# Optimization experiments

Measured on AMD Instinct MI355X. Metric: run time of the kernel, lower is better.

## Reference

```python
import jax, jax.numpy as jnp
import numpy as np

NUM_HEADS = 4
KERNEL = 4
EPS = 1e-6


def _causal_conv1d(x, w, b):
    # x: (B,S,D), w: (D,1,K) depthwise, b: (D,)
    xc = x.transpose(0, 2, 1)  # (B,D,S)
    y = jax.lax.conv_general_dilated(
        xc, w, window_strides=(1,), padding=[(w.shape[-1] - 1, 0)],
        feature_group_count=xc.shape[1])
    return (y + b[None, :, None]).transpose(0, 2, 1)  # (B,S,D)


def _headwise(x, w):
    # x: (B,S,D), w: (NH, DH_out, DH_in) block-diagonal linear, no bias
    B, S, D = x.shape
    nh, dout, din = w.shape
    xh = x.reshape(B, S, nh, din)
    return jnp.einsum('bshd,hod->bsho', xh, w).reshape(B, S, nh * dout)


def _slstm_scan(gates, R, b):
    # gates: (B,S,4,NH,DH) ordered [i,f,z,o]; R: (NH,DH,4*DH); b: (4,NH,DH)
    B, S, _, nh, dh = gates.shape
    gseq = gates.transpose(1, 0, 2, 3, 4)  # (S,B,4,NH,DH)
    zero = jnp.zeros((B, nh, dh), gates.dtype)
    init = (zero, zero, zero, zero)  # h, c, n, m

    def step(carry, g):
        h, c, n, m = carry
        rec = jnp.einsum('bhd,hdk->bhk', h, R)
        rec = rec.reshape(B, nh, 4, dh).transpose(0, 2, 1, 3)  # (B,4,NH,DH)
        raw = g + rec + b[None]
        iraw, fraw, zraw, oraw = raw[:, 0], raw[:, 1], raw[:, 2], raw[:, 3]
        logfplusm = m + jax.nn.log_sigmoid(fraw)
        m_new = jnp.maximum(iraw, logfplusm)  # stabilizer
        ig = jnp.exp(iraw - m_new)
        fg = jnp.exp(logfplusm - m_new)
        c_new = fg * c + ig * jnp.tanh(zraw)
        n_new = fg * n + ig
        h_new = jax.nn.sigmoid(oraw) * c_new / n_new
        return (h_new, c_new, n_new, m_new), h_new

    _, ys = jax.lax.scan(step, init, gseq)  # ys: (S,B,NH,DH)
    return ys.transpose(1, 2, 0, 3)  # (B,NH,S,DH)


def _multihead_layernorm(y, scale, bias):
    # y: (B,NH,S,DH); normalize over DH per head
    mu = y.mean(-1, keepdims=True)
    var = y.var(-1, keepdims=True)
    yn = (y - mu) * jax.lax.rsqrt(var + EPS)
    nh, dh = y.shape[1], y.shape[3]
    return yn * scale.reshape(1, nh, 1, dh) + bias.reshape(1, nh, 1, dh)


def setup_inputs() -> dict:
    key = jax.random.key(0)
    ks = jax.random.split(key, 12)
    B, S, D = 4, 2048, 1024
    nh, dh = NUM_HEADS, D // NUM_HEADS
    sd_conv = 1.0 / np.sqrt(KERNEL)
    sd_head = 1.0 / np.sqrt(dh)
    return {
        'x': jax.random.normal(ks[0], (B, S, D), jnp.float32),
        'conv_w': jax.random.normal(ks[1], (D, 1, KERNEL), jnp.float32) * sd_conv,
        'conv_b': jnp.zeros((D,), jnp.float32),
        'w_i': jax.random.normal(ks[2], (nh, dh, dh), jnp.float32) * sd_head,
        'w_f': jax.random.normal(ks[3], (nh, dh, dh), jnp.float32) * sd_head,
        'w_z': jax.random.normal(ks[4], (nh, dh, dh), jnp.float32) * sd_head,
        'w_o': jax.random.normal(ks[5], (nh, dh, dh), jnp.float32) * sd_head,
        'rec_kernel': jax.random.normal(ks[6], (nh, dh, 4 * dh), jnp.float32) * sd_head,
        'cell_bias': jnp.zeros((4, nh, dh), jnp.float32),
        'gn_scale': jnp.ones((D,), jnp.float32),
        'gn_bias': jnp.zeros((D,), jnp.float32),
    }


def reference(x, conv_w, conv_b, w_i, w_f, w_z, w_o, rec_kernel, cell_bias, gn_scale, gn_bias):
    B, S, D = x.shape
    dh = D // NUM_HEADS
    x_conv = jax.nn.swish(_causal_conv1d(x, conv_w, conv_b))
    i = _headwise(x_conv, w_i)
    f = _headwise(x_conv, w_f)
    z = _headwise(x, w_z)
    o = _headwise(x, w_o)
    # concat order [i,f,z,o]; reshape to (B,S,4,NH,DH)
    gates = jnp.stack([i, f, z, o], axis=2).reshape(B, S, 4, NUM_HEADS, dh)
    y = _slstm_scan(gates, rec_kernel, cell_bias)  # (B,NH,S,DH)
    out = _multihead_layernorm(y, gn_scale, gn_bias)
    return out.transpose(0, 2, 1, 3).reshape(B, S, D)
```

## Files before the change

kernel.cpp:

```cpp
#include <hip/hip_runtime.h>
#include <hip/hip_bf16.h>

#define NH 4
#define DH 256
#define DMODEL 1024
#define BB 4
#define SS 2048

typedef __attribute__((ext_vector_type(4))) float f32x4;
typedef __attribute__((ext_vector_type(8))) short bf16x8;
typedef __attribute__((ext_vector_type(4))) int i32x4;

__device__ __forceinline__ int dot4i8(int acc, int a, int b) {
#if __has_builtin(__builtin_amdgcn_sdot4)
    return __builtin_amdgcn_sdot4(a, b, acc, false);
#else
#pragma unroll
    for (int i = 0; i < 4; ++i) {
        int av = (a << (24 - 8 * i)) >> 24;
        int bv = (b << (24 - 8 * i)) >> 24;
        acc += av * bv;
    }
    return acc;
#endif
}

__global__ void k_conv(const float* __restrict__ x, const float* __restrict__ cw,
                       const float* __restrict__ cb, float* __restrict__ xc) {
    int bs = blockIdx.x;
    int s = bs & (SS - 1);
    const float* xrow = x + (size_t)bs * DMODEL;
#pragma unroll
    for (int dd = 0; dd < 4; ++dd) {
        int d = threadIdx.x + dd * 256;
        float w0 = cw[d * 4 + 0], w1 = cw[d * 4 + 1], w2 = cw[d * 4 + 2], w3 = cw[d * 4 + 3];
        float acc = cb[d] + w3 * xrow[d];
        if (s >= 1) acc += w2 * xrow[d - DMODEL];
        if (s >= 2) acc += w1 * xrow[d - 2 * DMODEL];
        if (s >= 3) acc += w0 * xrow[d - 3 * DMODEL];
        float sig = 1.f / (1.f + __expf(-acc));
        xc[(size_t)bs * DMODEL + d] = acc * sig;
    }
}

__global__ void k_gemm(const float* __restrict__ x, const float* __restrict__ xc,
                       const float* __restrict__ wi, const float* __restrict__ wf,
                       const float* __restrict__ wz, const float* __restrict__ wo,
                       float* __restrict__ gates) {
    int h = blockIdx.z >> 1, pair = blockIdx.z & 1;
    const float* A = pair ? x : xc;
    int n0 = blockIdx.y * 64;
    const float* W = (n0 < 256) ? (pair ? wz : wi) : (pair ? wo : wf);
    int nl = n0 & 255;
    int m0 = blockIdx.x * 64;

    __shared__ __align__(16) __hip_bfloat16 Al[64][72];
    __shared__ __align__(16) __hip_bfloat16 Bl[64][72];

    int tid = threadIdx.x;
    int lane = tid & 63, wv = tid >> 6;
    f32x4 acc[4] = {};

    for (int k0 = 0; k0 < 256; k0 += 64) {
        __syncthreads();
#pragma unroll
        for (int i = 0; i < 4; ++i) {
            int f4 = tid + i * 256;
            int r = f4 >> 4, c4 = (f4 & 15) * 4;
            const float* srcA = A + (size_t)(m0 + r) * DMODEL + h * DH + k0 + c4;
            float4 v = *(const float4*)srcA;
            Al[r][c4 + 0] = __float2bfloat16(v.x);
            Al[r][c4 + 1] = __float2bfloat16(v.y);
            Al[r][c4 + 2] = __float2bfloat16(v.z);
            Al[r][c4 + 3] = __float2bfloat16(v.w);
            const float* srcB = W + (size_t)(h * DH + nl + r) * DH + k0 + c4;
            float4 u = *(const float4*)srcB;
            Bl[r][c4 + 0] = __float2bfloat16(u.x);
            Bl[r][c4 + 1] = __float2bfloat16(u.y);
            Bl[r][c4 + 2] = __float2bfloat16(u.z);
            Bl[r][c4 + 3] = __float2bfloat16(u.w);
        }
        __syncthreads();
#pragma unroll
        for (int kk = 0; kk < 64; kk += 32) {
            bf16x8 a = *(const bf16x8*)&Al[wv * 16 + (lane & 15)][kk + (lane >> 4) * 8];
#pragma unroll
            for (int nt = 0; nt < 4; ++nt) {
                bf16x8 bfr = *(const bf16x8*)&Bl[nt * 16 + (lane & 15)][kk + (lane >> 4) * 8];
                acc[nt] = __builtin_amdgcn_mfma_f32_16x16x32_bf16(a, bfr, acc[nt], 0, 0, 0);
            }
        }
    }
#pragma unroll
    for (int nt = 0; nt < 4; ++nt)
#pragma unroll
        for (int r = 0; r < 4; ++r) {
            int m = m0 + wv * 16 + (lane >> 4) * 4 + r;
            int n = n0 + nt * 16 + (lane & 15);
            int b = m >> 11, s = m & (SS - 1);
            int g = pair * 2 + (n >> 8), d = n & 255;
            gates[((((size_t)(b * NH + h)) * SS + s) * 4 + g) * DH + d] = acc[nt][r];
        }
}

__global__ void k_prep(const float* __restrict__ R, int* __restrict__ Wq,
                       float* __restrict__ scales) {
    int colid = blockIdx.x * 4 + (threadIdx.x >> 6);
    int lane = threadIdx.x & 63;
    int h = colid >> 10, k = colid & 1023;
    const float* base = R + (size_t)h * 256 * 1024 + k;
    float v[4];
    float mx = 0.f;
#pragma unroll
    for (int i = 0; i < 4; ++i) {
        v[i] = base[(size_t)(lane * 4 + i) * 1024];
        mx = fmaxf(mx, fabsf(v[i]));
    }
    for (int off = 32; off; off >>= 1) mx = fmaxf(mx, __shfl_xor(mx, off));
    mx = fmaxf(mx, 1e-30f);
    float scale = mx * (1.f / 127.f);
    float inv = 127.f / mx;
    int pk = 0;
#pragma unroll
    for (int i = 0; i < 4; ++i) {
        int q = (int)rintf(v[i] * inv);
        q = max(-127, min(127, q));
        pk |= (q & 255) << (8 * i);
    }
    Wq[(h * 64 + lane) * 1024 + k] = pk;
    if (lane == 0) scales[h * 1024 + k] = scale;
}

__launch_bounds__(1024, 4)
__global__ void k_scan(const float* __restrict__ gates, const int* __restrict__ Wq,
                       const float* __restrict__ scales, const float* __restrict__ bias,
                       float* __restrict__ y) {
    int bh = blockIdx.x;
    int h = bh & 3;
    int t = threadIdx.x;

    __shared__ __align__(16) signed char hq[256];
    __shared__ float rec[1024];

    int w[64];
#pragma unroll
    for (int j = 0; j < 64; ++j) w[j] = Wq[(h * 64 + j) * 1024 + t];
    float colmul = scales[h * 1024 + t] * (1.f / 127.f);

    float c = 0.f, n = 0.f, mstate = 0.f;
    float bi = 0.f, bf_ = 0.f, bz = 0.f, bo = 0.f;
    int d = t;
    if (t < 256) {
        bi = bias[(0 * NH + h) * DH + d];
        bf_ = bias[(1 * NH + h) * DH + d];
        bz = bias[(2 * NH + h) * DH + d];
        bo = bias[(3 * NH + h) * DH + d];
    }
    if (t < 16) ((i32x4*)hq)[t] = (i32x4){0, 0, 0, 0};
    const float* gbase = gates + (size_t)bh * SS * 1024;
    float* ybase = y + (size_t)bh * SS * DH;
    __syncthreads();

    for (int s = 0; s < SS; ++s) {
        float gi = 0.f, gf = 0.f, gz = 0.f, go = 0.f;
        if (t < 256) {
            const float* gp = gbase + (size_t)s * 1024 + d;
            gi = gp[0]; gf = gp[256]; gz = gp[512]; go = gp[768];
        }
        int acc = 0;
#pragma unroll
        for (int g4 = 0; g4 < 4; ++g4) {
            i32x4 h0 = ((const i32x4*)hq)[g4 * 4 + 0];
            i32x4 h1 = ((const i32x4*)hq)[g4 * 4 + 1];
            i32x4 h2 = ((const i32x4*)hq)[g4 * 4 + 2];
            i32x4 h3 = ((const i32x4*)hq)[g4 * 4 + 3];
            acc = dot4i8(acc, w[g4 * 16 + 0], h0.x);
            acc = dot4i8(acc, w[g4 * 16 + 1], h0.y);
            acc = dot4i8(acc, w[g4 * 16 + 2], h0.z);
            acc = dot4i8(acc, w[g4 * 16 + 3], h0.w);
            acc = dot4i8(acc, w[g4 * 16 + 4], h1.x);
            acc = dot4i8(acc, w[g4 * 16 + 5], h1.y);
            acc = dot4i8(acc, w[g4 * 16 + 6], h1.z);
            acc = dot4i8(acc, w[g4 * 16 + 7], h1.w);
            acc = dot4i8(acc, w[g4 * 16 + 8], h2.x);
            acc = dot4i8(acc, w[g4 * 16 + 9], h2.y);
            acc = dot4i8(acc, w[g4 * 16 + 10], h2.z);
            acc = dot4i8(acc, w[g4 * 16 + 11], h2.w);
            acc = dot4i8(acc, w[g4 * 16 + 12], h3.x);
            acc = dot4i8(acc, w[g4 * 16 + 13], h3.y);
            acc = dot4i8(acc, w[g4 * 16 + 14], h3.z);
            acc = dot4i8(acc, w[g4 * 16 + 15], h3.w);
        }
        rec[t] = (float)acc * colmul;
        __syncthreads();
        if (t < 256) {
            float ri = rec[d], rf = rec[256 + d], rz = rec[512 + d], ro = rec[768 + d];
            float rawi = gi + ri + bi;
            float rawf = gf + rf + bf_;
            float rawz = gz + rz + bz;
            float rawo = go + ro + bo;
            float lsf = fminf(rawf, 0.f) - __logf(1.f + __expf(-fabsf(rawf)));
            float lfm = mstate + lsf;
            float mn = fmaxf(rawi, lfm);
            float ig = __expf(rawi - mn);
            float fg = __expf(lfm - mn);
            float az = fabsf(rawz);
            float e2 = __expf(-2.f * az);
            float th = (1.f - e2) / (1.f + e2);
            th = rawz < 0.f ? -th : th;
            c = fg * c + ig * th;
            n = fg * n + ig;
            mstate = mn;
            float so = 1.f / (1.f + __expf(-rawo));
            float hv = so * c / n;
            ybase[(size_t)s * DH + d] = hv;
            int q = (int)rintf(hv * 127.f);
            hq[d] = (signed char)q;
        }
        __syncthreads();
    }
}

__global__ void k_ln(const float* __restrict__ y, const float* __restrict__ gsc,
                     const float* __restrict__ gbi, float* __restrict__ out) {
    int bid = blockIdx.x;
    int s = bid & (SS - 1);
    int bh = bid >> 11;
    int b = bh >> 2, h = bh & 3;
    int d = threadIdx.x;
    float v = y[(size_t)bid * DH + d];
    float s1 = v, s2 = v * v;
    for (int off = 32; off; off >>= 1) {
        s1 += __shfl_xor(s1, off);
        s2 += __shfl_xor(s2, off);
    }
    __shared__ float a1[4], a2[4];
    int wv = threadIdx.x >> 6, ln = threadIdx.x & 63;
    if (ln == 0) { a1[wv] = s1; a2[wv] = s2; }
    __syncthreads();
    s1 = a1[0] + a1[1] + a1[2] + a1[3];
    s2 = a2[0] + a2[1] + a2[2] + a2[3];
    float mu = s1 * (1.f / 256.f);
    float var = s2 * (1.f / 256.f) - mu * mu;
    float rs = rsqrtf(var + 1e-6f);
    float o = (v - mu) * rs * gsc[h * DH + d] + gbi[h * DH + d];
    out[((size_t)(b * SS + s)) * DMODEL + h * DH + d] = o;
}

extern "C" void kernel_launch(void* const* d_in, const int* in_sizes, int n_in,
                              void* d_out, int out_size, void* d_ws, size_t ws_size,
                              hipStream_t stream) {
    (void)in_sizes; (void)n_in; (void)out_size; (void)ws_size;
    const float* x = (const float*)d_in[0];
    const float* cw = (const float*)d_in[1];
    const float* cb = (const float*)d_in[2];
    const float* wi = (const float*)d_in[3];
    const float* wf = (const float*)d_in[4];
    const float* wz = (const float*)d_in[5];
    const float* wo = (const float*)d_in[6];
    const float* R = (const float*)d_in[7];
    const float* cbias = (const float*)d_in[8];
    const float* gsc = (const float*)d_in[9];
    const float* gbi = (const float*)d_in[10];
    float* out = (float*)d_out;

    char* ws = (char*)d_ws;
    float* xc = (float*)ws;
    float* gates = (float*)(ws + 33554432ull);
    float* yb = (float*)(ws + 167772160ull);
    int* Wq = (int*)(ws + 201326592ull);
    float* scales = (float*)(ws + 202375168ull);

    k_prep<<<1024, 256, 0, stream>>>(R, Wq, scales);
    k_conv<<<BB * SS, 256, 0, stream>>>(x, cw, cb, xc);
    k_gemm<<<dim3(128, 8, 8), 256, 0, stream>>>(x, xc, wi, wf, wz, wo, gates);
    k_scan<<<16, 1024, 0, stream>>>(gates, Wq, scales, cbias, yb);
    k_ln<<<BB * SS * NH, 256, 0, stream>>>(yb, gsc, gbi, out);
}
```

Baseline: 2.107 ms.

## Interleave gate layout, prefetch next-step gates, split dot chains, lighten scan barriers

The GEMM epilogue now writes gates interleaved per channel as [d][4 gates], so the scan can load all four gates with one float4 per step. The scan loop also prefetches the next timestep's gates into registers a step ahead, to hide global load latency behind the recurrent dot products. The 64-long serial sdot4 chain is split into four independent accumulators to shorten the dependency chain. __syncthreads is replaced with a custom barrier that waits only on LDS counters (lgkmcnt), so the prefetched global load does not stall at the barrier. This relies on the barrier not needing vmcnt for correctness and changes the gate memory layout in two kernels together.

```diff
diff --git a/kernel.cpp b/kernel.cpp
--- a/kernel.cpp
+++ b/kernel.cpp
@@ -23,6 +23,13 @@
     }
     return acc;
 #endif
+}
+
+__device__ __forceinline__ void wg_barrier() {
+    __builtin_amdgcn_sched_barrier(0);
+    asm volatile("s_waitcnt lgkmcnt(0)" ::: "memory");
+    __builtin_amdgcn_s_barrier();
+    __builtin_amdgcn_sched_barrier(0);
 }
 
 __global__ void k_conv(const float* __restrict__ x, const float* __restrict__ cw,
@@ -99,7 +106,7 @@
             int n = n0 + nt * 16 + (lane & 15);
             int b = m >> 11, s = m & (SS - 1);
             int g = pair * 2 + (n >> 8), d = n & 255;
-            gates[((((size_t)(b * NH + h)) * SS + s) * 4 + g) * DH + d] = acc[nt][r];
+            gates[((((size_t)(b * NH + h)) * SS + s) * DH + d) * 4 + g] = acc[nt][r];
         }
 }
 
@@ -149,7 +156,7 @@
 
     float c = 0.f, n = 0.f, mstate = 0.f;
     float bi = 0.f, bf_ = 0.f, bz = 0.f, bo = 0.f;
-    int d = t;
+    int d = t & 255;
     if (t < 256) {
         bi = bias[(0 * NH + h) * DH + d];
         bf_ = bias[(1 * NH + h) * DH + d];
@@ -157,48 +164,51 @@
         bo = bias[(3 * NH + h) * DH + d];
     }
     if (t < 16) ((i32x4*)hq)[t] = (i32x4){0, 0, 0, 0};
-    const float* gbase = gates + (size_t)bh * SS * 1024;
+    const float4* gp = (const float4*)(gates + (size_t)bh * SS * 1024) + d;
     float* ybase = y + (size_t)bh * SS * DH;
     __syncthreads();
 
+    float4 gc = {0.f, 0.f, 0.f, 0.f};
+    if (t < 256) gc = gp[0];
+
     for (int s = 0; s < SS; ++s) {
-        float gi = 0.f, gf = 0.f, gz = 0.f, go = 0.f;
-        if (t < 256) {
-            const float* gp = gbase + (size_t)s * 1024 + d;
-            gi = gp[0]; gf = gp[256]; gz = gp[512]; go = gp[768];
-        }
-        int acc = 0;
+        float4 gn = gc;
+        if (t < 256 && s + 1 < SS) gn = gp[(size_t)(s + 1) * 256];
+
+        int accs[4];
 #pragma unroll
         for (int g4 = 0; g4 < 4; ++g4) {
             i32x4 h0 = ((const i32x4*)hq)[g4 * 4 + 0];
             i32x4 h1 = ((const i32x4*)hq)[g4 * 4 + 1];
             i32x4 h2 = ((const i32x4*)hq)[g4 * 4 + 2];
             i32x4 h3 = ((const i32x4*)hq)[g4 * 4 + 3];
-            acc = dot4i8(acc, w[g4 * 16 + 0], h0.x);
-            acc = dot4i8(acc, w[g4 * 16 + 1], h0.y);
-            acc = dot4i8(acc, w[g4 * 16 + 2], h0.z);
-            acc = dot4i8(acc, w[g4 * 16 + 3], h0.w);
-            acc = dot4i8(acc, w[g4 * 16 + 4], h1.x);
-            acc = dot4i8(acc, w[g4 * 16 + 5], h1.y);
-            acc = dot4i8(acc, w[g4 * 16 + 6], h1.z);
-            acc = dot4i8(acc, w[g4 * 16 + 7], h1.w);
-            acc = dot4i8(acc, w[g4 * 16 + 8], h2.x);
-            acc = dot4i8(acc, w[g4 * 16 + 9], h2.y);
-            acc = dot4i8(acc, w[g4 * 16 + 10], h2.z);
-            acc = dot4i8(acc, w[g4 * 16 + 11], h2.w);
-            acc = dot4i8(acc, w[g4 * 16 + 12], h3.x);
-            acc = dot4i8(acc, w[g4 * 16 + 13], h3.y);
-            acc = dot4i8(acc, w[g4 * 16 + 14], h3.z);
-            acc = dot4i8(acc, w[g4 * 16 + 15], h3.w);
-        }
-        rec[t] = (float)acc * colmul;
-        __syncthreads();
+            int a = 0;
+            a = dot4i8(a, w[g4 * 16 + 0], h0.x);
+            a = dot4i8(a, w[g4 * 16 + 1], h0.y);
+            a = dot4i8(a, w[g4 * 16 + 2], h0.z);
+            a = dot4i8(a, w[g4 * 16 + 3], h0.w);
+            a = dot4i8(a, w[g4 * 16 + 4], h1.x);
+            a = dot4i8(a, w[g4 * 16 + 5], h1.y);
+            a = dot4i8(a, w[g4 * 16 + 6], h1.z);
+            a = dot4i8(a, w[g4 * 16 + 7], h1.w);
+            a = dot4i8(a, w[g4 * 16 + 8], h2.x);
+            a = dot4i8(a, w[g4 * 16 + 9], h2.y);
+            a = dot4i8(a, w[g4 * 16 + 10], h2.z);
+            a = dot4i8(a, w[g4 * 16 + 11], h2.w);
+            a = dot4i8(a, w[g4 * 16 + 12], h3.x);
+            a = dot4i8(a, w[g4 * 16 + 13], h3.y);
+            a = dot4i8(a, w[g4 * 16 + 14], h3.z);
+            a = dot4i8(a, w[g4 * 16 + 15], h3.w);
+            accs[g4] = a;
+        }
+        rec[t] = (float)(accs[0] + accs[1] + accs[2] + accs[3]) * colmul;
+        wg_barrier();
         if (t < 256) {
             float ri = rec[d], rf = rec[256 + d], rz = rec[512 + d], ro = rec[768 + d];
-            float rawi = gi + ri + bi;
-            float rawf = gf + rf + bf_;
-            float rawz = gz + rz + bz;
-            float rawo = go + ro + bo;
+            float rawi = gc.x + ri + bi;
+            float rawf = gc.y + rf + bf_;
+            float rawz = gc.z + rz + bz;
+            float rawo = gc.w + ro + bo;
             float lsf = fminf(rawf, 0.f) - __logf(1.f + __expf(-fabsf(rawf)));
             float lfm = mstate + lsf;
             float mn = fmaxf(rawi, lfm);
@@ -217,7 +227,8 @@
             int q = (int)rintf(hv * 127.f);
             hq[d] = (signed char)q;
         }
-        __syncthreads();
+        gc = gn;
+        wg_barrier();
     }
 }
 
```

Result: slower. 2.246 ms (+6.6%).

## Restructure sLSTM scan: quad-split K reduction, double-buffered h, one barrier per step

Applied to the files above, without the earlier changes.

The recurrent scan now assigns four threads per hidden unit. Each thread computes a quarter of the K-dimension dot product for all four gates, and the partial sums are combined with DPP quad reductions instead of staging them in a shared `rec` array. The hidden state is double-buffered in LDS, which cuts the per-step sync to a single lightweight barrier. The next step's gate inputs are prefetched into registers. Every thread now runs the redundant elementwise cell math, and the barrier relies on a custom lgkmcnt wait.

```diff
diff --git a/kernel.cpp b/kernel.cpp
--- a/kernel.cpp
+++ b/kernel.cpp
@@ -23,6 +23,17 @@
     }
     return acc;
 #endif
+}
+
+__device__ __forceinline__ void wg_barrier() {
+    asm volatile("s_waitcnt lgkmcnt(0)" ::: "memory");
+    __builtin_amdgcn_s_barrier();
+}
+
+__device__ __forceinline__ int quad_reduce_add(int v) {
+    v += __builtin_amdgcn_update_dpp(0, v, 0xB1, 0xF, 0xF, true);
+    v += __builtin_amdgcn_update_dpp(0, v, 0x4E, 0xF, 0xF, true);
+    return v;
 }
 
 __global__ void k_conv(const float* __restrict__ x, const float* __restrict__ cw,
@@ -131,93 +142,106 @@
     if (lane == 0) scales[h * 1024 + k] = scale;
 }
 
-__launch_bounds__(1024, 4)
+__launch_bounds__(1024, 1)
 __global__ void k_scan(const float* __restrict__ gates, const int* __restrict__ Wq,
                        const float* __restrict__ scales, const float* __restrict__ bias,
                        float* __restrict__ y) {
     int bh = blockIdx.x;
     int h = bh & 3;
     int t = threadIdx.x;
-
-    __shared__ __align__(16) signed char hq[256];
-    __shared__ float rec[1024];
-
-    int w[64];
-#pragma unroll
-    for (int j = 0; j < 64; ++j) w[j] = Wq[(h * 64 + j) * 1024 + t];
-    float colmul = scales[h * 1024 + t] * (1.f / 127.f);
+    int d = t >> 2, q = t & 3;
+
+    __shared__ __align__(16) signed char hq[2][256];
+
+    int w[4][16];
+#pragma unroll
+    for (int g = 0; g < 4; ++g)
+#pragma unroll
+        for (int j = 0; j < 16; ++j)
+            w[g][j] = Wq[(h * 64 + q * 16 + j) * 1024 + g * 256 + d];
+
+    float colmul[4];
+#pragma unroll
+    for (int g = 0; g < 4; ++g)
+        colmul[g] = scales[h * 1024 + g * 256 + d] * (1.f / 127.f);
+
+    float bi = bias[(0 * NH + h) * DH + d];
+    float bf_ = bias[(1 * NH + h) * DH + d];
+    float bz = bias[(2 * NH + h) * DH + d];
+    float bo = bias[(3 * NH + h) * DH + d];
 
     float c = 0.f, n = 0.f, mstate = 0.f;
-    float bi = 0.f, bf_ = 0.f, bz = 0.f, bo = 0.f;
-    int d = t;
-    if (t < 256) {
-        bi = bias[(0 * NH + h) * DH + d];
-        bf_ = bias[(1 * NH + h) * DH + d];
-        bz = bias[(2 * NH + h) * DH + d];
-        bo = bias[(3 * NH + h) * DH + d];
-    }
-    if (t < 16) ((i32x4*)hq)[t] = (i32x4){0, 0, 0, 0};
-    const float* gbase = gates + (size_t)bh * SS * 1024;
-    float* ybase = y + (size_t)bh * SS * DH;
+    const float* gbase = gates + (size_t)bh * SS * 1024 + d;
+    float* ybase = y + (size_t)bh * SS * DH + d;
+
+    if (t < 32) ((i32x4*)hq)[t] = (i32x4){0, 0, 0, 0};
     __syncthreads();
 
+    float gcx = gbase[0], gcy = gbase[256], gcz = gbase[512], gcw = gbase[768];
+
+    int p = 0;
     for (int s = 0; s < SS; ++s) {
-        float gi = 0.f, gf = 0.f, gz = 0.f, go = 0.f;
-        if (t < 256) {
-            const float* gp = gbase + (size_t)s * 1024 + d;
-            gi = gp[0]; gf = gp[256]; gz = gp[512]; go = gp[768];
-        }
-        int acc = 0;
-#pragma unroll
-        for (int g4 = 0; g4 < 4; ++g4) {
-            i32x4 h0 = ((const i32x4*)hq)[g4 * 4 + 0];
-            i32x4 h1 = ((const i32x4*)hq)[g4 * 4 + 1];
-            i32x4 h2 = ((const i32x4*)hq)[g4 * 4 + 2];
-            i32x4 h3 = ((const i32x4*)hq)[g4 * 4 + 3];
-            acc = dot4i8(acc, w[g4 * 16 + 0], h0.x);
-            acc = dot4i8(acc, w[g4 * 16 + 1], h0.y);
-            acc = dot4i8(acc, w[g4 * 16 + 2], h0.z);
-            acc = dot4i8(acc, w[g4 * 16 + 3], h0.w);
-            acc = dot4i8(acc, w[g4 * 16 + 4], h1.x);
-            acc = dot4i8(acc, w[g4 * 16 + 5], h1.y);
-            acc = dot4i8(acc, w[g4 * 16 + 6], h1.z);
-            acc = dot4i8(acc, w[g4 * 16 + 7], h1.w);
-            acc = dot4i8(acc, w[g4 * 16 + 8], h2.x);
-            acc = dot4i8(acc, w[g4 * 16 + 9], h2.y);
-            acc = dot4i8(acc, w[g4 * 16 + 10], h2.z);
-            acc = dot4i8(acc, w[g4 * 16 + 11], h2.w);
-            acc = dot4i8(acc, w[g4 * 16 + 12], h3.x);
-            acc = dot4i8(acc, w[g4 * 16 + 13], h3.y);
-            acc = dot4i8(acc, w[g4 * 16 + 14], h3.z);
-            acc = dot4i8(acc, w[g4 * 16 + 15], h3.w);
-        }
-        rec[t] = (float)acc * colmul;
-        __syncthreads();
-        if (t < 256) {
-            float ri = rec[d], rf = rec[256 + d], rz = rec[512 + d], ro = rec[768 + d];
-            float rawi = gi + ri + bi;
-            float rawf = gf + rf + bf_;
-            float rawz = gz + rz + bz;
-            float rawo = go + ro + bo;
-            float lsf = fminf(rawf, 0.f) - __logf(1.f + __expf(-fabsf(rawf)));
-            float lfm = mstate + lsf;
-            float mn = fmaxf(rawi, lfm);
-            float ig = __expf(rawi - mn);
-            float fg = __expf(lfm - mn);
-            float az = fabsf(rawz);
-            float e2 = __expf(-2.f * az);
-            float th = (1.f - e2) / (1.f + e2);
-            th = rawz < 0.f ? -th : th;
-            c = fg * c + ig * th;
-            n = fg * n + ig;
-            mstate = mn;
-            float so = 1.f / (1.f + __expf(-rawo));
-            float hv = so * c / n;
-            ybase[(size_t)s * DH + d] = hv;
-            int q = (int)rintf(hv * 127.f);
-            hq[d] = (signed char)q;
-        }
-        __syncthreads();
+        float gnx = gcx, gny = gcy, gnz = gcz, gnw = gcw;
+        if (s + 1 < SS) {
+            const float* gp = gbase + (size_t)(s + 1) * 1024;
+            gnx = gp[0]; gny = gp[256]; gnz = gp[512]; gnw = gp[768];
+        }
+
+        const i32x4* hv4 = (const i32x4*)hq[p];
+        i32x4 h0 = hv4[q * 4 + 0];
+        i32x4 h1 = hv4[q * 4 + 1];
+        i32x4 h2 = hv4[q * 4 + 2];
+        i32x4 h3 = hv4[q * 4 + 3];
+        int hdw[16];
+        hdw[0] = h0.x; hdw[1] = h0.y; hdw[2] = h0.z; hdw[3] = h0.w;
+        hdw[4] = h1.x; hdw[5] = h1.y; hdw[6] = h1.z; hdw[7] = h1.w;
+        hdw[8] = h2.x; hdw[9] = h2.y; hdw[10] = h2.z; hdw[11] = h2.w;
+        hdw[12] = h3.x; hdw[13] = h3.y; hdw[14] = h3.z; hdw[15] = h3.w;
+
+        int acc[4] = {0, 0, 0, 0};
+#pragma unroll
+        for (int g = 0; g < 4; ++g)
+#pragma unroll
+            for (int j = 0; j < 16; ++j)
+                acc[g] = dot4i8(acc[g], w[g][j], hdw[j]);
+
+        acc[0] = quad_reduce_add(acc[0]);
+        acc[1] = quad_reduce_add(acc[1]);
+        acc[2] = quad_reduce_add(acc[2]);
+        acc[3] = quad_reduce_add(acc[3]);
+
+        float ri = (float)acc[0] * colmul[0];
+        float rf = (float)acc[1] * colmul[1];
+        float rz = (float)acc[2] * colmul[2];
+        float ro = (float)acc[3] * colmul[3];
+
+        float rawi = gcx + ri + bi;
+        float rawf = gcy + rf + bf_;
+        float rawz = gcz + rz + bz;
+        float rawo = gcw + ro + bo;
+        float lsf = fminf(rawf, 0.f) - __logf(1.f + __expf(-fabsf(rawf)));
+        float lfm = mstate + lsf;
+        float mn = fmaxf(rawi, lfm);
+        float ig = __expf(rawi - mn);
+        float fg = __expf(lfm - mn);
+        float az = fabsf(rawz);
+        float e2 = __expf(-2.f * az);
+        float th = (1.f - e2) / (1.f + e2);
+        th = rawz < 0.f ? -th : th;
+        c = fg * c + ig * th;
+        n = fg * n + ig;
+        mstate = mn;
+        float so = 1.f / (1.f + __expf(-rawo));
+        float hv = so * c / n;
+
+        if (q == 0) {
+            ybase[(size_t)s * DH] = hv;
+            hq[p ^ 1][d] = (signed char)(int)rintf(hv * 127.f);
+        }
+
+        gcx = gnx; gcy = gny; gcz = gnz; gcw = gnw;
+        p ^= 1;
+        wg_barrier();
     }
 }
 
```

Result: slower. 2.967 ms (+40.8%).

## Restructure sLSTM scan to 512 threads with lane-pair DPP exchange and one barrier

Applied to the files above, without the earlier changes.

The recurrent scan kernel now runs 512 threads per block, each computing two gate columns, so lane pairs hold all four gates for one hidden unit. The gates are exchanged with a DPP xor-1 swizzle instead of going through shared memory. A double-buffered quantized h vector removes one of the two workgroup barriers per step, and gate inputs are prefetched two steps ahead. The aim is to shorten the serial per-step critical path. The cost is twice the register-resident weights per thread and redundant activation math on both lanes of each pair.

```diff
diff --git a/kernel.cpp b/kernel.cpp
--- a/kernel.cpp
+++ b/kernel.cpp
@@ -23,6 +23,16 @@
     }
     return acc;
 #endif
+}
+
+__device__ __forceinline__ void wg_barrier() {
+    asm volatile("s_waitcnt lgkmcnt(0)" ::: "memory");
+    __builtin_amdgcn_s_barrier();
+}
+
+__device__ __forceinline__ float xor1_f32(float v) {
+    int r = __builtin_amdgcn_update_dpp(0, __float_as_int(v), 0xB1, 0xF, 0xF, true);
+    return __int_as_float(r);
 }
 
 __global__ void k_conv(const float* __restrict__ x, const float* __restrict__ cw,
@@ -131,94 +141,94 @@
     if (lane == 0) scales[h * 1024 + k] = scale;
 }
 
-__launch_bounds__(1024, 4)
+__launch_bounds__(512, 2)
 __global__ void k_scan(const float* __restrict__ gates, const int* __restrict__ Wq,
                        const float* __restrict__ scales, const float* __restrict__ bias,
                        float* __restrict__ y) {
     int bh = blockIdx.x;
     int h = bh & 3;
     int t = threadIdx.x;
-
-    __shared__ __align__(16) signed char hq[256];
-    __shared__ float rec[1024];
-
-    int w[64];
-#pragma unroll
-    for (int j = 0; j < 64; ++j) w[j] = Wq[(h * 64 + j) * 1024 + t];
-    float colmul = scales[h * 1024 + t] * (1.f / 127.f);
+    int d = t >> 1, pair = t & 1;
+
+    __shared__ __align__(16) signed char hq[2][256];
+
+    int col0 = pair * 256 + d;
+    int col1 = col0 + 512;
+
+    int w0[64], w1[64];
+#pragma unroll
+    for (int j = 0; j < 64; ++j) {
+        w0[j] = Wq[(h * 64 + j) * 1024 + col0];
+        w1[j] = Wq[(h * 64 + j) * 1024 + col1];
+    }
+    float cm0 = scales[h * 1024 + col0] * (1.f / 127.f);
+    float cm1 = scales[h * 1024 + col1] * (1.f / 127.f);
+    float b0 = bias[(pair * NH + h) * DH + d];
+    float b1 = bias[((2 + pair) * NH + h) * DH + d];
 
     float c = 0.f, n = 0.f, mstate = 0.f;
-    float bi = 0.f, bf_ = 0.f, bz = 0.f, bo = 0.f;
-    int d = t;
-    if (t < 256) {
-        bi = bias[(0 * NH + h) * DH + d];
-        bf_ = bias[(1 * NH + h) * DH + d];
-        bz = bias[(2 * NH + h) * DH + d];
-        bo = bias[(3 * NH + h) * DH + d];
-    }
-    if (t < 16) ((i32x4*)hq)[t] = (i32x4){0, 0, 0, 0};
     const float* gbase = gates + (size_t)bh * SS * 1024;
-    float* ybase = y + (size_t)bh * SS * DH;
+    float* ybase = y + (size_t)bh * SS * DH + d;
+
+    if (t < 32) ((i32x4*)hq)[t] = (i32x4){0, 0, 0, 0};
     __syncthreads();
 
-    for (int s = 0; s < SS; ++s) {
-        float gi = 0.f, gf = 0.f, gz = 0.f, go = 0.f;
-        if (t < 256) {
-            const float* gp = gbase + (size_t)s * 1024 + d;
-            gi = gp[0]; gf = gp[256]; gz = gp[512]; go = gp[768];
-        }
-        int acc = 0;
-#pragma unroll
-        for (int g4 = 0; g4 < 4; ++g4) {
-            i32x4 h0 = ((const i32x4*)hq)[g4 * 4 + 0];
-            i32x4 h1 = ((const i32x4*)hq)[g4 * 4 + 1];
-            i32x4 h2 = ((const i32x4*)hq)[g4 * 4 + 2];
-            i32x4 h3 = ((const i32x4*)hq)[g4 * 4 + 3];
-            acc = dot4i8(acc, w[g4 * 16 + 0], h0.x);
-            acc = dot4i8(acc, w[g4 * 16 + 1], h0.y);
-            acc = dot4i8(acc, w[g4 * 16 + 2], h0.z);
-            acc = dot4i8(acc, w[g4 * 16 + 3], h0.w);
-            acc = dot4i8(acc, w[g4 * 16 + 4], h1.x);
-            acc = dot4i8(acc, w[g4 * 16 + 5], h1.y);
-            acc = dot4i8(acc, w[g4 * 16 + 6], h1.z);
-            acc = dot4i8(acc, w[g4 * 16 + 7], h1.w);
-            acc = dot4i8(acc, w[g4 * 16 + 8], h2.x);
-            acc = dot4i8(acc, w[g4 * 16 + 9], h2.y);
-            acc = dot4i8(acc, w[g4 * 16 + 10], h2.z);
-            acc = dot4i8(acc, w[g4 * 16 + 11], h2.w);
-            acc = dot4i8(acc, w[g4 * 16 + 12], h3.x);
-            acc = dot4i8(acc, w[g4 * 16 + 13], h3.y);
-            acc = dot4i8(acc, w[g4 * 16 + 14], h3.z);
-            acc = dot4i8(acc, w[g4 * 16 + 15], h3.w);
-        }
-        rec[t] = (float)acc * colmul;
-        __syncthreads();
-        if (t < 256) {
-            float ri = rec[d], rf = rec[256 + d], rz = rec[512 + d], ro = rec[768 + d];
-            float rawi = gi + ri + bi;
-            float rawf = gf + rf + bf_;
-            float rawz = gz + rz + bz;
-            float rawo = go + ro + bo;
-            float lsf = fminf(rawf, 0.f) - __logf(1.f + __expf(-fabsf(rawf)));
-            float lfm = mstate + lsf;
-            float mn = fmaxf(rawi, lfm);
-            float ig = __expf(rawi - mn);
-            float fg = __expf(lfm - mn);
-            float az = fabsf(rawz);
-            float e2 = __expf(-2.f * az);
-            float th = (1.f - e2) / (1.f + e2);
-            th = rawz < 0.f ? -th : th;
-            c = fg * c + ig * th;
-            n = fg * n + ig;
-            mstate = mn;
-            float so = 1.f / (1.f + __expf(-rawo));
-            float hv = so * c / n;
-            ybase[(size_t)s * DH + d] = hv;
-            int q = (int)rintf(hv * 127.f);
-            hq[d] = (signed char)q;
-        }
-        __syncthreads();
-    }
+    float gA0 = gbase[col0], gA1 = gbase[col1];
+    float gB0 = gbase[1024 + col0], gB1 = gbase[1024 + col1];
+
+#define SCAN_STEP(P, G0, G1, SCUR)                                            \
+    {                                                                          \
+        int acc0 = 0, acc1 = 0;                                                \
+        const i32x4* hv4 = (const i32x4*)hq[P];                                \
+        _Pragma("unroll") for (int kb = 0; kb < 4; ++kb) {                     \
+            i32x4 ha = hv4[kb * 4 + 0];                                        \
+            i32x4 hb = hv4[kb * 4 + 1];                                        \
+            i32x4 hc = hv4[kb * 4 + 2];                                        \
+            i32x4 hd_ = hv4[kb * 4 + 3];                                       \
+            int hd[16] = {ha.x, ha.y, ha.z, ha.w, hb.x, hb.y, hb.z, hb.w,      \
+                          hc.x, hc.y, hc.z, hc.w, hd_.x, hd_.y, hd_.z, hd_.w}; \
+            _Pragma("unroll") for (int j = 0; j < 16; ++j) {                   \
+                acc0 = dot4i8(acc0, w0[kb * 16 + j], hd[j]);                   \
+                acc1 = dot4i8(acc1, w1[kb * 16 + j], hd[j]);                   \
+            }                                                                  \
+        }                                                                      \
+        float rawA = G0 + (float)acc0 * cm0 + b0;                              \
+        float rawB = G1 + (float)acc1 * cm1 + b1;                              \
+        int sp = (SCUR) + 2 < SS ? (SCUR) + 2 : SS - 1;                        \
+        G0 = gbase[(size_t)sp * 1024 + col0];                                  \
+        G1 = gbase[(size_t)sp * 1024 + col1];                                  \
+        float recvA = xor1_f32(rawA);                                          \
+        float recvB = xor1_f32(rawB);                                          \
+        float rawi = pair ? recvA : rawA;                                      \
+        float rawf = pair ? rawA : recvA;                                      \
+        float rawz = pair ? recvB : rawB;                                      \
+        float rawo = pair ? rawB : recvB;                                      \
+        float lsf = fminf(rawf, 0.f) - __logf(1.f + __expf(-fabsf(rawf)));     \
+        float lfm = mstate + lsf;                                              \
+        float mn = fmaxf(rawi, lfm);                                           \
+        float ig = __expf(rawi - mn);                                          \
+        float fg = __expf(lfm - mn);                                           \
+        float az = fabsf(rawz);                                                \
+        float e2 = __expf(-2.f * az);                                          \
+        float th = (1.f - e2) / (1.f + e2);                                    \
+        th = rawz < 0.f ? -th : th;                                            \
+        c = fg * c + ig * th;                                                  \
+        n = fg * n + ig;                                                       \
+        mstate = mn;                                                           \
+        float so = 1.f / (1.f + __expf(-rawo));                                \
+        float hv = so * c / n;                                                 \
+        if (!pair) {                                                           \
+            ybase[(size_t)(SCUR)*DH] = hv;                                     \
+            hq[(P) ^ 1][d] = (signed char)(int)rintf(hv * 127.f);              \
+        }                                                                      \
+        wg_barrier();                                                          \
+    }
+
+    for (int s = 0; s < SS; s += 2) {
+        SCAN_STEP(0, gA0, gA1, s)
+        SCAN_STEP(1, gB0, gB1, s + 1)
+    }
+#undef SCAN_STEP
 }
 
 __global__ void k_ln(const float* __restrict__ y, const float* __restrict__ gsc,
@@ -274,6 +284,6 @@
     k_prep<<<1024, 256, 0, stream>>>(R, Wq, scales);
     k_conv<<<BB * SS, 256, 0, stream>>>(x, cw, cb, xc);
     k_gemm<<<dim3(128, 8, 8), 256, 0, stream>>>(x, xc, wi, wf, wz, wo, gates);
-    k_scan<<<16, 1024, 0, stream>>>(gates, Wq, scales, cbias, yb);
+    k_scan<<<16, 512, 0, stream>>>(gates, Wq, scales, cbias, yb);
     k_ln<<<BB * SS * NH, 256, 0, stream>>>(yb, gsc, gbi, out);
 }
```

After: 2.136 ms. Within noise of the previous version (+1.4%).
